# Kernel optimization log

Measured on AMD Instinct MI355X. Metric: run time of the kernel, lower is better.

## Reference

```python
import jax, jax.numpy as jnp
import numpy as np

THETA = 10.0      # spike threshold
TAU_SR = 10.0     # synaptic (PSP) alpha-kernel time constant
TAU_REF = 1.0     # refractory alpha-kernel time constant
SCALE_REF = 2.0   # refractory scale (kernel = -scaleRef*theta*(t/tauRef)e^{1-t/tauRef})
TAU_RHO = 1.0     # surrogate-gradient width
SCALE_RHO = 1.0   # surrogate-gradient scale
TS = 1.0          # simulation step (ms)
E = 2.718281828459045

@jax.custom_vjp
def spike_surrogate(u):
    return (u >= THETA).astype(u.dtype)

def _spike_fwd(u):
    return (u >= THETA).astype(u.dtype), u

def _spike_bwd(u, g):
    # SLAYER surrogate spike-pdf gradient
    pdf = (SCALE_RHO / TAU_RHO) * jnp.exp(-jnp.abs(u - THETA) / TAU_RHO)
    return (g * pdf,)

spike_surrogate.defvjp(_spike_fwd, _spike_bwd)

def psp_spike(x):
    # x: (N, ..., T). PSP = causal temporal conv with alpha kernel
    # eps(t) = (t/tauSr) e^{1-t/tauSr}, realized EXACTLY as a 2-state IIR recursion.
    # spike = threshold; each emitted spike injects refractory alpha kernel
    # -scaleRef*theta*(t/tauRef) e^{1-t/tauRef} into the future membrane.
    xt = jnp.moveaxis(x, -1, 0)  # (T, ...)
    a_sr = jnp.exp(jnp.asarray(-TS / TAU_SR, x.dtype))
    a_rf = jnp.exp(jnp.asarray(-TS / TAU_REF, x.dtype))
    c_sr = E / TAU_SR
    c_rf = -SCALE_REF * THETA * E / TAU_REF
    z = jnp.zeros_like(xt[0])
    def step(carry, xi):
        gp, hp, gr, hr = carry
        hp = a_sr * (hp + gp)
        gp = a_sr * gp + xi
        hr = a_rf * (hr + gr)   # same recursion over past spikes
        gr = a_rf * gr
        u = c_sr * hp + c_rf * hr  # membrane = PSP + refractory
        s = spike_surrogate(u)
        return (gp, hp, gr + s, hr), s
    _, st = jax.lax.scan(step, (z, z, z, z), xt)
    return jnp.moveaxis(st, 0, -1)

def sum_pool(x, k):
    # SLAYER pool: conv with constant weight 1.1*theta over kxk window, stride k
    N, C, H, W, T = x.shape
    xs = x.reshape(N, C, H // k, k, W // k, k, T).sum(axis=(3, 5))
    return 1.1 * THETA * xs

def conv2dt(x, w, pad):
    # SLAYER conv = conv3d with kernel (k,k,1): per-time-step 2D conv, T as trailing dim
    return jax.lax.conv_general_dilated(
        x, w[..., None], (1, 1, 1),
        [(pad, pad), (pad, pad), (0, 0)],
        dimension_numbers=('NCHWT', 'OIHWT', 'NCHWT'))

def forward(s_in, w1, w2, w3, w4a, w4b):
    x = psp_spike(sum_pool(s_in, 4))              # (N,2,32,32,T)
    x = psp_spike(conv2dt(x, w1, 2))              # (N,32,32,32,T)
    x = psp_spike(sum_pool(x, 2))                 # (N,32,16,16,T)
    x = psp_spike(conv2dt(x, w2, 1))              # (N,64,16,16,T)
    x = psp_spike(sum_pool(x, 2))                 # (N,64,8,8,T)
    x = psp_spike(conv2dt(x, w3, 1))              # (N,64,8,8,T)
    N, T = x.shape[0], x.shape[-1]
    xf = x.reshape(N, -1, T)                      # (N, 64*8*8, T)
    x = psp_spike(jnp.einsum('nft,of->not', xf, w4a))  # (N,256,T)
    x = psp_spike(jnp.einsum('nct,oc->not', x, w4b))   # (N,11,T)
    return x

def setup_inputs():
    key = jax.random.key(0)
    ks = jax.random.split(key, 6)
    N, T = 4, 300
    # Bernoulli(0.05) event spikes, DVS128 gesture format (N,2,128,128,T)
    s_in = (jax.random.uniform(ks[0], (N, 2, 128, 128, T)) < 0.05).astype(jnp.float32)
    w1 = jax.random.normal(ks[1], (32, 2, 5, 5), jnp.float32) * 10.0 * 0.05   # weightScale=10
    w2 = jax.random.normal(ks[2], (64, 32, 3, 3), jnp.float32) * 20.0 * 0.01  # weightScale=20
    w3 = jax.random.normal(ks[3], (64, 64, 3, 3), jnp.float32) * 20.0 * 0.01  # weightScale=20
    w4a = jax.random.normal(ks[4], (256, 64 * 8 * 8), jnp.float32) * 0.01
    w4b = jax.random.normal(ks[5], (11, 256), jnp.float32) * 0.05
    return {"s_in": s_in, "w1": w1, "w2": w2, "w3": w3, "w4a": w4a, "w4b": w4b}

def reference(s_in, w1, w2, w3, w4a, w4b):
    return forward(s_in, w1, w2, w3, w4a, w4b)
```

## Files before the change

kernel.cpp:

```cpp
#include <hip/hip_runtime.h>
#include <cstdint>

#define TT 300
#define TC 75
#define NBATCH 4

typedef float pf2 __attribute__((ext_vector_type(2)));
typedef _Float16 h8t __attribute__((ext_vector_type(8)));
typedef float f32x4 __attribute__((ext_vector_type(4)));

__device__ __forceinline__ void psp_step(float z, float& gp, float& hp, float& gr, float& hr, float& s_out) {
    hp = 0.90483741803595957f * (hp + gp);
    gp = 0.90483741803595957f * gp + z;
    hr = 0.36787944117144233f * (hr + gr);
    gr = 0.36787944117144233f * gr;
    float u = 0.27182818284590452f * hp + (-54.365636569180904f) * hr;
    float s = (u >= 10.0f) ? 1.0f : 0.0f;
    gr += s;
    s_out = s;
}

template <int R>
__global__ void k_scan_redp(const float* __restrict__ z, float* __restrict__ s,
                            int n_neur, int pstride) {
    int i = blockIdx.x * 64 + threadIdx.x;
    if (i >= n_neur) return;
    const float* zp = z + (size_t)i * TT;
    float* sp = s + (size_t)i * TT;
    float gp = 0.f, hp = 0.f, gr = 0.f, hr = 0.f;
#pragma unroll 1
    for (int c = 0; c < 25; ++c) {
        const float* p = zp + c * 12;
        float4 a0 = *(const float4*)(p);
        float4 a1 = *(const float4*)(p + 4);
        float4 a2 = *(const float4*)(p + 8);
#pragma unroll
        for (int r = 1; r < R; ++r) {
            const float* pr = p + (size_t)r * pstride;
            float4 b0 = *(const float4*)(pr);
            float4 b1 = *(const float4*)(pr + 4);
            float4 b2 = *(const float4*)(pr + 8);
            a0.x += b0.x; a0.y += b0.y; a0.z += b0.z; a0.w += b0.w;
            a1.x += b1.x; a1.y += b1.y; a1.z += b1.z; a1.w += b1.w;
            a2.x += b2.x; a2.y += b2.y; a2.z += b2.z; a2.w += b2.w;
        }
        float4 o0, o1, o2;
        psp_step(a0.x, gp, hp, gr, hr, o0.x);
        psp_step(a0.y, gp, hp, gr, hr, o0.y);
        psp_step(a0.z, gp, hp, gr, hr, o0.z);
        psp_step(a0.w, gp, hp, gr, hr, o0.w);
        psp_step(a1.x, gp, hp, gr, hr, o1.x);
        psp_step(a1.y, gp, hp, gr, hr, o1.y);
        psp_step(a1.z, gp, hp, gr, hr, o1.z);
        psp_step(a1.w, gp, hp, gr, hr, o1.w);
        psp_step(a2.x, gp, hp, gr, hr, o2.x);
        psp_step(a2.y, gp, hp, gr, hr, o2.y);
        psp_step(a2.z, gp, hp, gr, hr, o2.z);
        psp_step(a2.w, gp, hp, gr, hr, o2.w);
        float* q = sp + c * 12;
        *(float4*)(q) = o0;
        *(float4*)(q + 4) = o1;
        *(float4*)(q + 8) = o2;
    }
}

__global__ void k_scan16_f16(const float* __restrict__ z, _Float16* __restrict__ s16) {
    int i = blockIdx.x * 64 + threadIdx.x;
    int n = i >> 12, f = i & 4095;
    const float* zp = z + (size_t)i * 16;
    _Float16* sp = s16 + ((size_t)n * TT) * 4096 + f;
    float gp = 0.f, hp = 0.f, gr = 0.f, hr = 0.f;
#define SC16_CHUNK(TCI, NTT) do {                                              \
    const float* pp = zp + (size_t)(TCI) * (16384 * 16);                       \
    float4 a0 = *(const float4*)(pp);                                          \
    float4 a1 = *(const float4*)(pp + 4);                                      \
    float4 a2 = *(const float4*)(pp + 8);                                      \
    float4 a3 = *(const float4*)(pp + 12);                                     \
    float zv[16] = {a0.x,a0.y,a0.z,a0.w,a1.x,a1.y,a1.z,a1.w,                   \
                    a2.x,a2.y,a2.z,a2.w,a3.x,a3.y,a3.z,a3.w};                  \
    _Pragma("unroll")                                                          \
    for (int tt = 0; tt < (NTT); ++tt) {                                       \
        float o;                                                               \
        psp_step(zv[tt], gp, hp, gr, hr, o);                                   \
        sp[(size_t)((TCI) * 16 + tt) * 4096] = (_Float16)o;                    \
    }                                                                          \
} while (0)
#pragma unroll 1
    for (int tcc = 0; tcc < 18; ++tcc) SC16_CHUNK(tcc, 16);
    SC16_CHUNK(18, 12);
#undef SC16_CHUNK
}

template <int C, int H2, int W2>
__global__ void __launch_bounds__(256) k_spsq16(const float* __restrict__ z,
                                                _Float16* __restrict__ s16) {
    constexpr int H = 2 * H2, W = 2 * W2;
    constexpr int NP = NBATCH * C * H * W;
    constexpr int C8 = C / 8;
    __shared__ _Float16 tile[16 * C];

    int i = blockIdx.x * 256 + threadIdx.x;
    int q = i & 3;
    int p = i >> 2;
    int c  = p % C;
    int x2 = (p / C) % W2;
    int y2 = (p / (C * W2)) % H2;
    int n  = p / (C * W2 * H2);
    int dy = q >> 1, dx = q & 1;
    int pz = ((n * C + c) * H + 2 * y2 + dy) * W + 2 * x2 + dx;
    const float* zp = z + (size_t)pz * 16;

    int tid = threadIdx.x;
    int wt  = tid & 15;
    int wc8 = tid >> 4;
    int p0 = blockIdx.x * 64;
    int wx2 = (p0 / C) % W2;
    int wy2 = (p0 / (C * W2)) % H2;
    int wn  = p0 / (C * W2 * H2);
    _Float16* wbase = s16 + ((((size_t)(wn * C8 + wc8) * H2 + wy2) * W2 + wx2) * TT) * 8;

    float gp = 0.f, hp = 0.f, gr = 0.f, hr = 0.f;
    float Gp = 0.f, Hp = 0.f, Gr = 0.f, Hr = 0.f;
#define SPSQ_CHUNK(TCI, NTT) do {                                              \
    const float* pp = zp + (size_t)(TCI) * (NP * 16);                          \
    float4 a0 = *(const float4*)(pp);                                          \
    float4 a1 = *(const float4*)(pp + 4);                                      \
    float4 a2 = *(const float4*)(pp + 8);                                      \
    float4 a3 = *(const float4*)(pp + 12);                                     \
    float zv[16] = {a0.x,a0.y,a0.z,a0.w,a1.x,a1.y,a1.z,a1.w,                   \
                    a2.x,a2.y,a2.z,a2.w,a3.x,a3.y,a3.z,a3.w};                  \
    float ov[16];                                                              \
    _Pragma("unroll")                                                          \
    for (int tt = 0; tt < (NTT); ++tt) {                                       \
        float sq;                                                              \
        psp_step(zv[tt], gp, hp, gr, hr, sq);                                  \
        float t1 = sq + __shfl_xor(sq, 1, 64);                                 \
        float pool = t1 + __shfl_xor(t1, 2, 64);                               \
        psp_step(11.0f * pool, Gp, Hp, Gr, Hr, ov[tt]);                        \
    }                                                                          \
    __syncthreads();                                                           \
    if (q == 0) {                                                              \
        _Pragma("unroll")                                                      \
        for (int tt = 0; tt < (NTT); ++tt)                                     \
            tile[tt * C + c] = (_Float16)ov[tt];                               \
    }                                                                          \
    __syncthreads();                                                           \
    if (tid < 16 * C8 && wt < (NTT)) {                                         \
        h8t v = *(const h8t*)(tile + wt * C + wc8 * 8);                        \
        *(h8t*)(wbase + (size_t)((TCI) * 16 + wt) * 8) = v;                    \
    }                                                                          \
} while (0)
#pragma unroll 1
    for (int tcc = 0; tcc < 18; ++tcc) SPSQ_CHUNK(tcc, 16);
    SPSQ_CHUNK(18, 12);
#undef SPSQ_CHUNK
}

__global__ void k_pack_wmfma(const float* __restrict__ w, _Float16* __restrict__ wm,
                             int CIN, int COUT, int total) {
    int i = blockIdx.x * 256 + threadIdx.x;
    if (i >= total) return;
    int lane = i & 63;
    int r = i >> 6;
    int ver = r & 1; r >>= 1;
    int KC = CIN >> 5, CT = COUT >> 4;
    int ct = r % CT; r /= CT;
    int kc = r % KC;
    int tap = r / KC;
    int ky = tap / 3, kx = tap % 3;
    int co  = ct * 16 + (lane & 15);
    int ci0 = kc * 32 + (lane >> 4) * 8;
    _Float16 out[8];
#pragma unroll
    for (int j = 0; j < 8; ++j) {
        float wf = w[((co * CIN + ci0 + j) * 3 + ky) * 3 + kx];
        _Float16 hi = (_Float16)wf;
        out[j] = ver ? (_Float16)((wf - (float)hi) * 4096.0f) : hi;
    }
    *(h8t*)(wm + (size_t)i * 8) = *(h8t*)out;
}

__global__ void k_pack_wfc(const float* __restrict__ w, _Float16* __restrict__ wm,
                           int FIN, int COUT, int total) {
    int i = blockIdx.x * 256 + threadIdx.x;
    if (i >= total) return;
    int lane = i & 63;
    int r = i >> 6;
    int ver = r & 1; r >>= 1;
    int CT = COUT >> 4;
    int ct = r % CT;
    int kg = r / CT;
    int co = ct * 16 + (lane & 15);
    int f0 = kg * 32 + (lane >> 4) * 8;
    _Float16 out[8];
#pragma unroll
    for (int j = 0; j < 8; ++j) {
        float wf = w[(size_t)co * FIN + f0 + j];
        _Float16 hi = (_Float16)wf;
        out[j] = ver ? (_Float16)((wf - (float)hi) * 4096.0f) : hi;
    }
    *(h8t*)(wm + (size_t)i * 8) = *(h8t*)out;
}

__global__ void k_pack_wl1(const float* __restrict__ w, _Float16* __restrict__ wm) {
    int i = blockIdx.x * 256 + threadIdx.x;
    if (i >= 768) return;
    int lane = i & 63;
    int r = i >> 6;
    int ver = r & 1;
    int ch = (r >> 1) & 1;
    int kc = r >> 2;
    int co = ch * 16 + (lane & 15);
    int k0 = kc * 32 + (lane >> 4) * 8;
    _Float16 out[8];
#pragma unroll
    for (int j = 0; j < 8; ++j) {
        int k = k0 + j;
        int ky = k >> 4, slot = k & 15, kx = slot >> 1, ci = slot & 1;
        float wf = (ky < 5 && kx < 5) ? w[((co * 2 + ci) * 5 + ky) * 5 + kx] : 0.f;
        _Float16 hif = (_Float16)wf;
        out[j] = ver ? (_Float16)((wf - (float)hif) * 4096.0f) : hif;
    }
    *(h8t*)(wm + (size_t)i * 8) = *(h8t*)out;
}

__global__ void k_pool4(const float* __restrict__ x, float* __restrict__ z) {
    int idx = blockIdx.x * 256 + threadIdx.x;
    if (idx >= NBATCH * 2 * 32 * 32 * TC) return;
    int tc = idx % TC;
    int p  = idx / TC;
    int w  = p % 32;
    int h  = (p / 32) % 32;
    int nc = p / (32 * 32);
    const float* base = x + (((size_t)nc * 128 + h * 4) * 128 + w * 4) * TT + tc * 4;
    float ax = 0.f, ay = 0.f, az = 0.f, aw = 0.f;
#pragma unroll
    for (int i = 0; i < 4; ++i)
#pragma unroll
        for (int j = 0; j < 4; ++j) {
            float4 v = *(const float4*)(base + ((size_t)i * 128 + j) * TT);
            ax += v.x; ay += v.y; az += v.z; aw += v.w;
        }
    float4 o; o.x = 11.0f * ax; o.y = 11.0f * ay; o.z = 11.0f * az; o.w = 11.0f * aw;
    *(float4*)(z + (size_t)p * TT + tc * 4) = o;
}

__global__ void __launch_bounds__(256) k_l1_fused(const float* __restrict__ s0,
                                                  const _Float16* __restrict__ wl1,
                                                  _Float16* __restrict__ s2h) {
    constexpr int NT = 19;
    __shared__ _Float16 stage[7 * 16 * 42];
    __shared__ float    trans[256 * 17];
    __shared__ _Float16 tile[4 * 16 * 16];

    int bid = blockIdx.x;
    int y2 = bid & 15;
    int xh = (bid >> 4) & 3;
    int ch = (bid >> 6) & 1;
    int n  = bid >> 7;
    int tid = threadIdx.x;
    int lane = tid & 63;
    int wv = tid >> 6;
    int tl = lane & 15;
    int hi = lane >> 4;
    int yy = wv >> 1;
    int xq = wv & 1;

    int q    = tid & 3;
    int co_s = (tid >> 2) & 15;
    int x2l_s = tid >> 6;
    int wt  = tid & 15;
    int wc8 = (tid >> 4) & 1;
    int wx  = tid >> 5;

    bool   it_v[4];
    size_t it_off[4];
    int    it_adr[4];
    int    it_tq[4];
#pragma unroll
    for (int ii = 0; ii < 4; ++ii) {
        int i = tid + ii * 256;
        int tq = i & 3;
        int lx = (i >> 2) & 15;
        int ci = (i >> 6) & 1;
        int r  = i >> 7;
        int gx = xh * 8 + lx - 2;
        int gy = y2 * 2 + r - 2;
        bool sp = (i < 896) && gx >= 0 && gx < 32 && gy >= 0 && gy < 32;
        it_v[ii]   = sp;
        it_off[ii] = sp ? ((((size_t)(n * 2 + ci) * 32 + gy) * 32 + gx) * TT + tq * 4) : 0;
        it_adr[ii] = (r * 16 + tq * 4) * 42 + lx * 2 + ci;
        it_tq[ii]  = tq;
    }

    const h8t* wv4 = (const h8t*)wl1;
    h8t wfr[3][2];
#pragma unroll
    for (int kc = 0; kc < 3; ++kc) {
        wfr[kc][0] = wv4[((kc * 2 + ch) * 2 + 0) * 64 + lane];
        wfr[kc][1] = wv4[((kc * 2 + ch) * 2 + 1) * 64 + lane];
    }

    float gp = 0.f, hp = 0.f, gr = 0.f, hr = 0.f;
    float Gp = 0.f, Hp = 0.f, Gr = 0.f, Hr = 0.f;

    float4 pf[4];
#pragma unroll
    for (int ii = 0; ii < 4; ++ii) {
        pf[ii] = make_float4(0.f, 0.f, 0.f, 0.f);
        if (it_v[ii]) pf[ii] = *(const float4*)(s0 + it_off[ii]);
    }

#pragma unroll 1
    for (int tc = 0; tc < NT; ++tc) {
#pragma unroll
        for (int ii = 0; ii < 4; ++ii) {
            if (tid + ii * 256 < 896) {
                stage[it_adr[ii] + 0 * 42] = (_Float16)pf[ii].x;
                stage[it_adr[ii] + 1 * 42] = (_Float16)pf[ii].y;
                stage[it_adr[ii] + 2 * 42] = (_Float16)pf[ii].z;
                stage[it_adr[ii] + 3 * 42] = (_Float16)pf[ii].w;
            }
        }
        if (tc + 1 < NT) {
#pragma unroll
            for (int ii = 0; ii < 4; ++ii) {
                float4 v = make_float4(0.f, 0.f, 0.f, 0.f);
                if (it_v[ii] && (tc + 1) * 16 + it_tq[ii] * 4 + 3 < TT)
                    v = *(const float4*)(s0 + it_off[ii] + (tc + 1) * 16);
                pf[ii] = v;
            }
        }
        __syncthreads();
        f32x4 ah4[4], al4[4];
#pragma unroll
        for (int xi = 0; xi < 4; ++xi) { ah4[xi] = (f32x4){0.f,0.f,0.f,0.f}; al4[xi] = (f32x4){0.f,0.f,0.f,0.f}; }
#pragma unroll
        for (int kc = 0; kc < 3; ++kc) {
            int row = yy + 2 * kc + (hi >> 1);
#pragma unroll
            for (int xi = 0; xi < 4; ++xi) {
                int xo = xq * 4 + xi;
                const uint32_t* lp = (const uint32_t*)(stage + (row * 16 + tl) * 42 + xo * 2 + (hi & 1) * 8);
                union { uint32_t u[4]; h8t h; } bu;
                bu.u[0] = lp[0]; bu.u[1] = lp[1]; bu.u[2] = lp[2]; bu.u[3] = lp[3];
                ah4[xi] = __builtin_amdgcn_mfma_f32_16x16x32_f16(wfr[kc][0], bu.h, ah4[xi], 0, 0, 0);
                al4[xi] = __builtin_amdgcn_mfma_f32_16x16x32_f16(wfr[kc][1], bu.h, al4[xi], 0, 0, 0);
            }
        }
#pragma unroll
        for (int xi = 0; xi < 4; ++xi) {
            int xo = xq * 4 + xi;
#pragma unroll
            for (int r = 0; r < 4; ++r) {
                float u = ah4[xi][r] + al4[xi][r] * 2.44140625e-4f;
                int rowt = ((xo >> 1) * 16 + hi * 4 + r) * 4 + yy * 2 + (xo & 1);
                trans[rowt * 17 + tl] = u;
            }
        }
        __syncthreads();
#pragma unroll
        for (int t = 0; t < 16; ++t) {
            float u = trans[tid * 17 + t];
            float sq;
            psp_step(u, gp, hp, gr, hr, sq);
            float t1 = sq + __shfl_xor(sq, 1, 64);
            float pool = t1 + __shfl_xor(t1, 2, 64);
            float ov;
            psp_step(11.0f * pool, Gp, Hp, Gr, Hr, ov);
            if (q == 0) tile[(x2l_s * 16 + t) * 16 + co_s] = (_Float16)ov;
        }
        __syncthreads();
        if (tid < 128) {
            int tg = tc * 16 + wt;
            if (tg < TT) {
                h8t v = *(const h8t*)(tile + (wx * 16 + wt) * 16 + wc8 * 8);
                int cg8 = ch * 2 + wc8;
                int x2g = xh * 4 + wx;
                *(h8t*)(s2h + ((((size_t)(n * 4 + cg8) * 16 + y2) * 16 + x2g) * (size_t)TT + tg) * 8) = v;
            }
        }
    }
}

template <int CIN, int COUT, int H, int W, int YPB, int XSPL>
__global__ void __launch_bounds__(256, 2) k_conv_mfma(const _Float16* __restrict__ s16,
                                                      const _Float16* __restrict__ wm,
                                                      float* __restrict__ z) {
    constexpr int NT = 19;
    constexpr int KC = CIN / 32;
    constexpr int CH = CIN / 8;
    constexpr int XW = W / XSPL;
    constexpr int XL = XW + 2;
    constexpr int CT = COUT / 16;
    constexpr int XPW = XW / 4;
    constexpr int ROWS = YPB + 2;
    constexpr int NP = NBATCH * COUT * H * W;
    __shared__ _Float16 lds[ROWS * XL * 16 * CIN];

    int bid = blockIdx.x;
    int tc = bid % NT;
    int r0 = bid / NT;
    int yb = (r0 % (H / YPB)) * YPB;
    r0 /= (H / YPB);
    int xh = r0 % XSPL;
    int n  = r0 / XSPL;
    int xb = xh * XW;
    int tid = threadIdx.x;

    constexpr int TOT = ROWS * XL * CH * 16;
    for (int i = tid; i < TOT; i += 256) {
        int t   = i & 15;
        int c   = (i >> 4) % CH;
        int xc  = ((i >> 4) / CH) % XL;
        int row = ((i >> 4) / CH) / XL;
        int tg = tc * 16 + t;
        int xi = xb + xc - 1;
        int yi = yb + row - 1;
        h8t v;
#pragma unroll
        for (int e = 0; e < 8; ++e) v[e] = (_Float16)0.0f;
        if (xi >= 0 && xi < W && yi >= 0 && yi < H && tg < TT)
            v = *(const h8t*)(s16 + ((((size_t)(n * CH + c) * H + yi) * W + xi) * TT + tg) * 8);
        int swz = (CIN == 32) ? ((t >> 1) & 3) : (t & 7);
        int off = ((row * XL + xc) * 16 + t) * CIN + ((c ^ swz) << 3);
        *(h8t*)(lds + off) = v;
    }
    __syncthreads();

    int lane = tid & 63;
    int wv   = tid >> 6;
    int tl   = lane & 15;
    int hi   = lane >> 4;
    const h8t* wmv = (const h8t*)wm;
    int swz = (CIN == 32) ? ((tl >> 1) & 3) : (tl & 7);

#pragma unroll
    for (int yy = 0; yy < YPB; ++yy) {
        f32x4 acc_h[XPW][CT], acc_l[XPW][CT];
#pragma unroll
        for (int a = 0; a < XPW; ++a)
#pragma unroll
            for (int b = 0; b < CT; ++b) {
                acc_h[a][b] = (f32x4){0.f, 0.f, 0.f, 0.f};
                acc_l[a][b] = (f32x4){0.f, 0.f, 0.f, 0.f};
            }
#pragma unroll
        for (int ky = 0; ky < 3; ++ky) {
#pragma unroll
            for (int kx = 0; kx < 3; ++kx) {
                int tap = ky * 3 + kx;
#pragma unroll
                for (int kc = 0; kc < KC; ++kc) {
                    h8t bf[XPW];
#pragma unroll
                    for (int xi = 0; xi < XPW; ++xi) {
                        int x = wv * XPW + xi;
                        int c = kc * 4 + hi;
                        int off = (((yy + ky) * XL + (x + kx)) * 16 + tl) * CIN + ((c ^ swz) << 3);
                        bf[xi] = *(const h8t*)(lds + off);
                    }
#pragma unroll
                    for (int ct = 0; ct < CT; ++ct) {
                        size_t wbase = ((size_t)(tap * KC + kc) * CT + ct) * 2;
                        h8t ah = wmv[(wbase + 0) * 64 + lane];
                        h8t al = wmv[(wbase + 1) * 64 + lane];
#pragma unroll
                        for (int xi = 0; xi < XPW; ++xi) {
                            acc_h[xi][ct] = __builtin_amdgcn_mfma_f32_16x16x32_f16(ah, bf[xi], acc_h[xi][ct], 0, 0, 0);
                            acc_l[xi][ct] = __builtin_amdgcn_mfma_f32_16x16x32_f16(al, bf[xi], acc_l[xi][ct], 0, 0, 0);
                        }
                    }
                }
            }
        }
#pragma unroll
        for (int xi = 0; xi < XPW; ++xi) {
            int x = xb + wv * XPW + xi;
#pragma unroll
            for (int ct = 0; ct < CT; ++ct) {
#pragma unroll
                for (int r = 0; r < 4; ++r) {
                    int co = ct * 16 + hi * 4 + r;
                    int pz = ((n * COUT + co) * H + (yb + yy)) * W + x;
                    z[((size_t)tc * NP + pz) * 16 + tl]
                        = acc_h[xi][ct][r] + acc_l[xi][ct][r] * 2.44140625e-4f;
                }
            }
        }
    }
}

template <int FIN, int OUT>
__global__ void __launch_bounds__(256) k_fc_mfma(const _Float16* __restrict__ s16,
                                                 const _Float16* __restrict__ wm,
                                                 float* __restrict__ z) {
    constexpr int NT = 19;
    constexpr int CT = OUT / 16;
    constexpr int KCH = 512;
    constexpr int NK = FIN / KCH;
    __shared__ _Float16 lds[KCH * 16];

    int bid = blockIdx.x;
    int tc = bid % NT;
    int n  = (bid / NT) % NBATCH;
    int cg = bid / (NT * NBATCH);
    int tid = threadIdx.x;
    int lane = tid & 63, wv = tid >> 6;
    int tl = lane & 15, hi = lane >> 4;
    int ct = cg * 4 + wv;

    f32x4 acc_h = (f32x4){0.f, 0.f, 0.f, 0.f};
    f32x4 acc_l = (f32x4){0.f, 0.f, 0.f, 0.f};
    const h8t* wmv = (const h8t*)wm;

    for (int kb = 0; kb < NK; ++kb) {
        __syncthreads();
#pragma unroll
        for (int j = 0; j < 4; ++j) {
            int chunk = tid + j * 256;
            int c = chunk & 63;
            int t = chunk >> 6;
            int tg = tc * 16 + t;
            h8t v;
#pragma unroll
            for (int e = 0; e < 8; ++e) v[e] = (_Float16)0.0f;
            if (tg < TT) v = *(const h8t*)(s16 + ((size_t)(n * TT + tg) * FIN + kb * KCH + c * 8));
            *(h8t*)(lds + ((t * 64 + (c ^ (t & 7))) << 3)) = v;
        }
        __syncthreads();
#pragma unroll
        for (int kc = 0; kc < KCH / 32; ++kc) {
            int c = kc * 4 + hi;
            h8t bf = *(const h8t*)(lds + ((tl * 64 + (c ^ (tl & 7))) << 3));
            size_t wbase = ((size_t)((kb * (KCH / 32) + kc) * CT + ct)) * 2;
            h8t ah = wmv[(wbase + 0) * 64 + lane];
            h8t al = wmv[(wbase + 1) * 64 + lane];
            acc_h = __builtin_amdgcn_mfma_f32_16x16x32_f16(ah, bf, acc_h, 0, 0, 0);
            acc_l = __builtin_amdgcn_mfma_f32_16x16x32_f16(al, bf, acc_l, 0, 0, 0);
        }
    }
    int tg = tc * 16 + tl;
    if (tg < TT) {
#pragma unroll
        for (int r = 0; r < 4; ++r) {
            int co = ct * 16 + hi * 4 + r;
            z[(size_t)(n * OUT + co) * TT + tg] = acc_h[r] + acc_l[r] * 2.44140625e-4f;
        }
    }
}

template <int OUT, int FIN, int OPER, int FSPLIT>
__global__ void k_fc_a(const float* __restrict__ s, const float* __restrict__ wgt,
                       float* __restrict__ z) {
    constexpr int OG = OUT / OPER, FCH = FIN / FSPLIT;
    int idx = blockIdx.x * 256 + threadIdx.x;
    if (idx >= NBATCH * OG * TC * FSPLIT) return;
    int tc = idx % TC;
    int og = (idx / TC) % OG;
    int n  = (idx / (TC * OG)) % NBATCH;
    int sp = idx / (TC * OG * NBATCH);
    const float* sb = s + (size_t)n * FIN * TT + (size_t)sp * FCH * TT + tc * 4;
    const float* wb = wgt + (size_t)sp * FCH;
    pf2 acc[OPER][2];
#pragma unroll
    for (int k = 0; k < OPER; ++k) { acc[k][0] = (pf2){0.f, 0.f}; acc[k][1] = (pf2){0.f, 0.f}; }
#pragma unroll 2
    for (int f = 0; f < FCH; f += 4) {
        float4 s0 = *(const float4*)(sb + (size_t)(f + 0) * TT);
        float4 s1 = *(const float4*)(sb + (size_t)(f + 1) * TT);
        float4 s2 = *(const float4*)(sb + (size_t)(f + 2) * TT);
        float4 s3 = *(const float4*)(sb + (size_t)(f + 3) * TT);
        pf2 s0a = {s0.x, s0.y}, s0b = {s0.z, s0.w};
        pf2 s1a = {s1.x, s1.y}, s1b = {s1.z, s1.w};
        pf2 s2a = {s2.x, s2.y}, s2b = {s2.z, s2.w};
        pf2 s3a = {s3.x, s3.y}, s3b = {s3.z, s3.w};
#pragma unroll
        for (int k = 0; k < OPER; ++k) {
            float4 wv = *(const float4*)(wb + (size_t)(og * OPER + k) * FIN + f);
            pf2 wx = {wv.x, wv.x}, wy = {wv.y, wv.y}, wz = {wv.z, wv.z}, ww = {wv.w, wv.w};
            pf2 a0 = acc[k][0], a1 = acc[k][1];
            a0 = __builtin_elementwise_fma(wx, s0a, a0);
            a0 = __builtin_elementwise_fma(wy, s1a, a0);
            a0 = __builtin_elementwise_fma(wz, s2a, a0);
            a0 = __builtin_elementwise_fma(ww, s3a, a0);
            a1 = __builtin_elementwise_fma(wx, s0b, a1);
            a1 = __builtin_elementwise_fma(wy, s1b, a1);
            a1 = __builtin_elementwise_fma(wz, s2b, a1);
            a1 = __builtin_elementwise_fma(ww, s3b, a1);
            acc[k][0] = a0; acc[k][1] = a1;
        }
    }
#pragma unroll
    for (int k = 0; k < OPER; ++k) {
        float4 o;
        o.x = acc[k][0].x; o.y = acc[k][0].y; o.z = acc[k][1].x; o.w = acc[k][1].y;
        *(float4*)(z + ((size_t)sp * NBATCH * OUT + (size_t)n * OUT + og * OPER + k) * TT + tc * 4) = o;
    }
}

extern "C" void kernel_launch(void* const* d_in, const int* in_sizes, int n_in,
                              void* d_out, int out_size, void* d_ws, size_t ws_size,
                              hipStream_t stream) {
    const float* s_in = (const float*)d_in[0];
    const float* w1   = (const float*)d_in[1];
    const float* w2   = (const float*)d_in[2];
    const float* w3   = (const float*)d_in[3];
    const float* w4a  = (const float*)d_in[4];
    const float* w4b  = (const float*)d_in[5];
    float* out = (float*)d_out;

    float* Z  = (float*)d_ws;
    float* Sb = Z + 39321600;
    float* WP = Sb + 9830400;
    _Float16* wm2 = (_Float16*)(WP + 1600);
    _Float16* wm3 = (_Float16*)(WP + 1600 + 18432);
    _Float16* S16 = (_Float16*)(Z + 25000000);
    _Float16* wm4 = (_Float16*)(Z + 28000000);
    _Float16* wl1m = (_Float16*)(Z + 30000000);
    float* s0 = Sb;
    _Float16* s2h = (_Float16*)(Sb + 2500000);
    _Float16* s4h = (_Float16*)(Sb + 5000000);

    auto g = [](int n) { return (n + 255) / 256; };
    auto g64 = [](int n) { return (n + 63) / 64; };

    k_pack_wl1<<<3, 256, 0, stream>>>(w1, wl1m);
    k_pack_wmfma<<<g(4608), 256, 0, stream>>>(w2, wm2, 32, 64, 4608);
    k_pack_wmfma<<<g(9216), 256, 0, stream>>>(w3, wm3, 64, 64, 9216);
    k_pack_wfc<<<g(262144), 256, 0, stream>>>(w4a, wm4, 4096, 256, 262144);

    k_pool4<<<g(614400), 256, 0, stream>>>(s_in, Z);
    k_scan_redp<1><<<g64(8192), 64, 0, stream>>>(Z, s0, 8192, 0);

    k_l1_fused<<<512, 256, 0, stream>>>(s0, wl1m, s2h);

    k_conv_mfma<32, 64, 16, 16, 2, 2><<<1216, 256, 0, stream>>>(s2h, wm2, Z);
    k_spsq16<64, 8, 8><<<256, 256, 0, stream>>>(Z, s4h);

    k_conv_mfma<64, 64, 8, 8, 1, 2><<<1216, 256, 0, stream>>>(s4h, wm3, Z);
    k_scan16_f16<<<256, 64, 0, stream>>>(Z, S16);

    k_fc_mfma<4096, 256><<<304, 256, 0, stream>>>(S16, wm4, Z);
    k_scan_redp<1><<<g64(1024), 64, 0, stream>>>(Z, Sb, 1024, 0);

    k_fc_a<11, 256, 1, 1><<<g(3300), 256, 0, stream>>>(Sb, w4b, Z);
    k_scan_redp<1><<<1, 64, 0, stream>>>(Z, out, 44, 0);
}
```

Baseline: 523.0 us.

## Merge weight-pack kernels and double the time chunk in fused layer-1 kernel

The four weight-packing kernels become one launch that dispatches on a flat index, removing three launch overheads. The fused layer-1 conv/PSP/pool kernel now processes 32 time steps per chunk instead of 16. This halves the number of chunk iterations and barriers, and each thread now loads all 7 input rows with a simpler index map. The cost is larger shared memory and more accumulator registers, which may limit occupancy despite the launch_bounds hint of 2 blocks per CU.

```diff
diff --git a/kernel.cpp b/kernel.cpp
--- a/kernel.cpp
+++ b/kernel.cpp
@@ -156,10 +156,8 @@
 #undef SPSQ_CHUNK
 }
 
-__global__ void k_pack_wmfma(const float* __restrict__ w, _Float16* __restrict__ wm,
-                             int CIN, int COUT, int total) {
-    int i = blockIdx.x * 256 + threadIdx.x;
-    if (i >= total) return;
+__device__ __forceinline__ void pack_wmfma_item(int i, const float* __restrict__ w,
+                                                _Float16* __restrict__ wm, int CIN, int COUT) {
     int lane = i & 63;
     int r = i >> 6;
     int ver = r & 1; r >>= 1;
@@ -180,10 +178,8 @@
     *(h8t*)(wm + (size_t)i * 8) = *(h8t*)out;
 }
 
-__global__ void k_pack_wfc(const float* __restrict__ w, _Float16* __restrict__ wm,
-                           int FIN, int COUT, int total) {
-    int i = blockIdx.x * 256 + threadIdx.x;
-    if (i >= total) return;
+__device__ __forceinline__ void pack_wfc_item(int i, const float* __restrict__ w,
+                                              _Float16* __restrict__ wm, int FIN, int COUT) {
     int lane = i & 63;
     int r = i >> 6;
     int ver = r & 1; r >>= 1;
@@ -202,9 +198,8 @@
     *(h8t*)(wm + (size_t)i * 8) = *(h8t*)out;
 }
 
-__global__ void k_pack_wl1(const float* __restrict__ w, _Float16* __restrict__ wm) {
-    int i = blockIdx.x * 256 + threadIdx.x;
-    if (i >= 768) return;
+__device__ __forceinline__ void pack_wl1_item(int i, const float* __restrict__ w,
+                                              _Float16* __restrict__ wm) {
     int lane = i & 63;
     int r = i >> 6;
     int ver = r & 1;
@@ -222,6 +217,17 @@
         out[j] = ver ? (_Float16)((wf - (float)hif) * 4096.0f) : hif;
     }
     *(h8t*)(wm + (size_t)i * 8) = *(h8t*)out;
+}
+
+__global__ void k_pack_all(const float* __restrict__ w1, const float* __restrict__ w2,
+                           const float* __restrict__ w3, const float* __restrict__ w4a,
+                           _Float16* __restrict__ wl1m, _Float16* __restrict__ wm2,
+                           _Float16* __restrict__ wm3, _Float16* __restrict__ wm4) {
+    int i = blockIdx.x * 256 + threadIdx.x;
+    if (i < 768)          pack_wl1_item(i, w1, wl1m);
+    else if (i < 5376)    pack_wmfma_item(i - 768, w2, wm2, 32, 64);
+    else if (i < 14592)   pack_wmfma_item(i - 5376, w3, wm3, 64, 64);
+    else if (i < 276736)  pack_wfc_item(i - 14592, w4a, wm4, 4096, 256);
 }
 
 __global__ void k_pool4(const float* __restrict__ x, float* __restrict__ z) {
@@ -245,13 +251,13 @@
     *(float4*)(z + (size_t)p * TT + tc * 4) = o;
 }
 
-__global__ void __launch_bounds__(256) k_l1_fused(const float* __restrict__ s0,
-                                                  const _Float16* __restrict__ wl1,
-                                                  _Float16* __restrict__ s2h) {
-    constexpr int NT = 19;
-    __shared__ _Float16 stage[7 * 16 * 42];
-    __shared__ float    trans[256 * 17];
-    __shared__ _Float16 tile[4 * 16 * 16];
+__global__ void __launch_bounds__(256, 2) k_l1_fused(const float* __restrict__ s0,
+                                                     const _Float16* __restrict__ wl1,
+                                                     _Float16* __restrict__ s2h) {
+    constexpr int NT = 10;
+    __shared__ _Float16 stage[7 * 32 * 42];
+    __shared__ float    trans[256 * 33];
+    __shared__ _Float16 tile[4 * 32 * 16];
 
     int bid = blockIdx.x;
     int y2 = bid & 15;
@@ -266,32 +272,20 @@
     int yy = wv >> 1;
     int xq = wv & 1;
 
-    int q    = tid & 3;
-    int co_s = (tid >> 2) & 15;
+    int q     = tid & 3;
+    int co_s  = (tid >> 2) & 15;
     int x2l_s = tid >> 6;
-    int wt  = tid & 15;
-    int wc8 = (tid >> 4) & 1;
-    int wx  = tid >> 5;
-
-    bool   it_v[4];
-    size_t it_off[4];
-    int    it_adr[4];
-    int    it_tq[4];
-#pragma unroll
-    for (int ii = 0; ii < 4; ++ii) {
-        int i = tid + ii * 256;
-        int tq = i & 3;
-        int lx = (i >> 2) & 15;
-        int ci = (i >> 6) & 1;
-        int r  = i >> 7;
-        int gx = xh * 8 + lx - 2;
-        int gy = y2 * 2 + r - 2;
-        bool sp = (i < 896) && gx >= 0 && gx < 32 && gy >= 0 && gy < 32;
-        it_v[ii]   = sp;
-        it_off[ii] = sp ? ((((size_t)(n * 2 + ci) * 32 + gy) * 32 + gx) * TT + tq * 4) : 0;
-        it_adr[ii] = (r * 16 + tq * 4) * 42 + lx * 2 + ci;
-        it_tq[ii]  = tq;
-    }
+    int wt  = tid & 31;
+    int wc8 = (tid >> 5) & 1;
+    int wx  = tid >> 6;
+
+    int tq = tid & 7;
+    int lx = (tid >> 3) & 15;
+    int ci = tid >> 7;
+    int gx = xh * 8 + lx - 2;
+    bool gxok = (gx >= 0 && gx < 32);
+    size_t boff = (((size_t)(n * 2 + ci) * 32) * 32 + (gxok ? gx : 0)) * TT + tq * 4;
+    int adr0 = (tq * 4) * 42 + lx * 2 + ci;
 
     const h8t* wv4 = (const h8t*)wl1;
     h8t wfr[3][2];
@@ -304,77 +298,89 @@
     float gp = 0.f, hp = 0.f, gr = 0.f, hr = 0.f;
     float Gp = 0.f, Hp = 0.f, Gr = 0.f, Hr = 0.f;
 
-    float4 pf[4];
-#pragma unroll
-    for (int ii = 0; ii < 4; ++ii) {
+    float4 pf[7];
+#pragma unroll
+    for (int ii = 0; ii < 7; ++ii) {
+        int gy = y2 * 2 + ii - 2;
         pf[ii] = make_float4(0.f, 0.f, 0.f, 0.f);
-        if (it_v[ii]) pf[ii] = *(const float4*)(s0 + it_off[ii]);
+        if (gxok && gy >= 0 && gy < 32)
+            pf[ii] = *(const float4*)(s0 + boff + (size_t)gy * (32 * TT));
     }
 
 #pragma unroll 1
     for (int tc = 0; tc < NT; ++tc) {
 #pragma unroll
-        for (int ii = 0; ii < 4; ++ii) {
-            if (tid + ii * 256 < 896) {
-                stage[it_adr[ii] + 0 * 42] = (_Float16)pf[ii].x;
-                stage[it_adr[ii] + 1 * 42] = (_Float16)pf[ii].y;
-                stage[it_adr[ii] + 2 * 42] = (_Float16)pf[ii].z;
-                stage[it_adr[ii] + 3 * 42] = (_Float16)pf[ii].w;
-            }
+        for (int ii = 0; ii < 7; ++ii) {
+            int a = adr0 + ii * (32 * 42);
+            stage[a + 0 * 42] = (_Float16)pf[ii].x;
+            stage[a + 1 * 42] = (_Float16)pf[ii].y;
+            stage[a + 2 * 42] = (_Float16)pf[ii].z;
+            stage[a + 3 * 42] = (_Float16)pf[ii].w;
         }
         if (tc + 1 < NT) {
 #pragma unroll
-            for (int ii = 0; ii < 4; ++ii) {
+            for (int ii = 0; ii < 7; ++ii) {
+                int gy = y2 * 2 + ii - 2;
                 float4 v = make_float4(0.f, 0.f, 0.f, 0.f);
-                if (it_v[ii] && (tc + 1) * 16 + it_tq[ii] * 4 + 3 < TT)
-                    v = *(const float4*)(s0 + it_off[ii] + (tc + 1) * 16);
+                if (gxok && gy >= 0 && gy < 32 && (tc + 1) * 32 + tq * 4 + 3 < TT)
+                    v = *(const float4*)(s0 + boff + (size_t)gy * (32 * TT) + (tc + 1) * 32);
                 pf[ii] = v;
             }
         }
         __syncthreads();
-        f32x4 ah4[4], al4[4];
-#pragma unroll
-        for (int xi = 0; xi < 4; ++xi) { ah4[xi] = (f32x4){0.f,0.f,0.f,0.f}; al4[xi] = (f32x4){0.f,0.f,0.f,0.f}; }
+        f32x4 ah4[2][4], al4[2][4];
+#pragma unroll
+        for (int tg = 0; tg < 2; ++tg)
+#pragma unroll
+            for (int xi = 0; xi < 4; ++xi) {
+                ah4[tg][xi] = (f32x4){0.f, 0.f, 0.f, 0.f};
+                al4[tg][xi] = (f32x4){0.f, 0.f, 0.f, 0.f};
+            }
 #pragma unroll
         for (int kc = 0; kc < 3; ++kc) {
-            int row = yy + 2 * kc + (hi >> 1);
+            int rowb = yy + 2 * kc + (hi >> 1);
+#pragma unroll
+            for (int tg = 0; tg < 2; ++tg) {
+#pragma unroll
+                for (int xi = 0; xi < 4; ++xi) {
+                    int xo = xq * 4 + xi;
+                    const uint32_t* lp = (const uint32_t*)(stage + (rowb * 32 + tg * 16 + tl) * 42 + xo * 2 + (hi & 1) * 8);
+                    union { uint32_t u[4]; h8t h; } bu;
+                    bu.u[0] = lp[0]; bu.u[1] = lp[1]; bu.u[2] = lp[2]; bu.u[3] = lp[3];
+                    ah4[tg][xi] = __builtin_amdgcn_mfma_f32_16x16x32_f16(wfr[kc][0], bu.h, ah4[tg][xi], 0, 0, 0);
+                    al4[tg][xi] = __builtin_amdgcn_mfma_f32_16x16x32_f16(wfr[kc][1], bu.h, al4[tg][xi], 0, 0, 0);
+                }
+            }
+        }
+#pragma unroll
+        for (int tg = 0; tg < 2; ++tg)
 #pragma unroll
             for (int xi = 0; xi < 4; ++xi) {
                 int xo = xq * 4 + xi;
-                const uint32_t* lp = (const uint32_t*)(stage + (row * 16 + tl) * 42 + xo * 2 + (hi & 1) * 8);
-                union { uint32_t u[4]; h8t h; } bu;
-                bu.u[0] = lp[0]; bu.u[1] = lp[1]; bu.u[2] = lp[2]; bu.u[3] = lp[3];
-                ah4[xi] = __builtin_amdgcn_mfma_f32_16x16x32_f16(wfr[kc][0], bu.h, ah4[xi], 0, 0, 0);
-                al4[xi] = __builtin_amdgcn_mfma_f32_16x16x32_f16(wfr[kc][1], bu.h, al4[xi], 0, 0, 0);
-            }
-        }
-#pragma unroll
-        for (int xi = 0; xi < 4; ++xi) {
-            int xo = xq * 4 + xi;
-#pragma unroll
-            for (int r = 0; r < 4; ++r) {
-                float u = ah4[xi][r] + al4[xi][r] * 2.44140625e-4f;
-                int rowt = ((xo >> 1) * 16 + hi * 4 + r) * 4 + yy * 2 + (xo & 1);
-                trans[rowt * 17 + tl] = u;
-            }
-        }
+#pragma unroll
+                for (int r = 0; r < 4; ++r) {
+                    float u = ah4[tg][xi][r] + al4[tg][xi][r] * 2.44140625e-4f;
+                    int rowt = ((xo >> 1) * 16 + hi * 4 + r) * 4 + yy * 2 + (xo & 1);
+                    trans[rowt * 33 + tg * 16 + tl] = u;
+                }
+            }
         __syncthreads();
 #pragma unroll
-        for (int t = 0; t < 16; ++t) {
-            float u = trans[tid * 17 + t];
+        for (int t = 0; t < 32; ++t) {
+            float u = trans[tid * 33 + t];
             float sq;
             psp_step(u, gp, hp, gr, hr, sq);
             float t1 = sq + __shfl_xor(sq, 1, 64);
             float pool = t1 + __shfl_xor(t1, 2, 64);
             float ov;
             psp_step(11.0f * pool, Gp, Hp, Gr, Hr, ov);
-            if (q == 0) tile[(x2l_s * 16 + t) * 16 + co_s] = (_Float16)ov;
+            if (q == 0) tile[(x2l_s * 32 + t) * 16 + co_s] = (_Float16)ov;
         }
         __syncthreads();
-        if (tid < 128) {
-            int tg = tc * 16 + wt;
+        {
+            int tg = tc * 32 + wt;
             if (tg < TT) {
-                h8t v = *(const h8t*)(tile + (wx * 16 + wt) * 16 + wc8 * 8);
+                h8t v = *(const h8t*)(tile + (wx * 32 + wt) * 16 + wc8 * 8);
                 int cg8 = ch * 2 + wc8;
                 int x2g = xh * 4 + wx;
                 *(h8t*)(s2h + ((((size_t)(n * 4 + cg8) * 16 + y2) * 16 + x2g) * (size_t)TT + tg) * 8) = v;
@@ -625,10 +631,7 @@
     auto g = [](int n) { return (n + 255) / 256; };
     auto g64 = [](int n) { return (n + 63) / 64; };
 
-    k_pack_wl1<<<3, 256, 0, stream>>>(w1, wl1m);
-    k_pack_wmfma<<<g(4608), 256, 0, stream>>>(w2, wm2, 32, 64, 4608);
-    k_pack_wmfma<<<g(9216), 256, 0, stream>>>(w3, wm3, 64, 64, 9216);
-    k_pack_wfc<<<g(262144), 256, 0, stream>>>(w4a, wm4, 4096, 256, 262144);
+    k_pack_all<<<g(276736), 256, 0, stream>>>(w1, w2, w3, w4a, wl1m, wm2, wm3, wm4);
 
     k_pool4<<<g(614400), 256, 0, stream>>>(s_in, Z);
     k_scan_redp<1><<<g64(8192), 64, 0, stream>>>(Z, s0, 8192, 0);
```

Result: no change. 518.4 us (-0.9%).
